# Optimization experiments

Hardware: AMD Instinct MI355X
Metric: run time of the kernel (lower is better)

Reference implementation:

```python
import jax, jax.numpy as jnp
import numpy as np

N = 8192
IN_DIM = 256
HID = 512
NUM_CLASSES = 256
AVG_DEG = 32


def setup_inputs() -> dict:
    key = jax.random.key(0)
    k_a, k_x, k_w1, k_w2 = jax.random.split(key, 4)
    # Binary adjacency with avg degree ~AVG_DEG (entries are exactly 1.0, matching
    # A.nonzero() edge extraction with implicit unit edge weights).
    A = (jax.random.uniform(k_a, (N, N)) < (AVG_DEG / N)).astype(jnp.float32)
    x = jax.random.normal(k_x, (N, IN_DIM), dtype=jnp.float32)
    # GCNConv params: glorot-ish weights, zero bias.
    W1 = jax.random.normal(k_w1, (IN_DIM, HID), dtype=jnp.float32) / np.sqrt(IN_DIM)
    b1 = jnp.zeros((HID,), dtype=jnp.float32)
    W2 = jax.random.normal(k_w2, (HID, NUM_CLASSES), dtype=jnp.float32) / np.sqrt(HID)
    b2 = jnp.zeros((NUM_CLASSES,), dtype=jnp.float32)
    sigmoid_param = jnp.array([10.0], dtype=jnp.float32)
    return {"A": A, "x": x, "W1": W1, "b1": b1, "W2": W2, "b2": b2,
            "sigmoid_param": sigmoid_param}


def _gcn_propagate(A, deg_inv_sqrt, h):
    # PyG GCNConv aggregation with self-loops, without materializing A + I:
    # out_j = d_j^{-1/2} * sum_i A_ij d_i^{-1/2} h_i  +  d_j^{-1} h_j
    m = deg_inv_sqrt[:, None] * h              # [N, d]
    agg = A.T @ m                              # messages flow row -> col
    return deg_inv_sqrt[:, None] * agg + (deg_inv_sqrt[:, None] ** 2) * h


def reference(A, x, W1, b1, W2, b2, sigmoid_param):
    # Degree from column sums of (A + I) — matches gcn_norm's scatter on col.
    deg = jnp.sum(A, axis=0) + 1.0             # [N], >= 1 thanks to self-loop
    deg_inv_sqrt = jax.lax.rsqrt(deg)
    skip_x = x                                  # nn.Identity skip connection
    # GCNConv 1: linear then normalized aggregation, then bias; ReLU.
    h = _gcn_propagate(A, deg_inv_sqrt, x @ W1) + b1
    h = jax.nn.relu(h)
    # GCNConv 2.
    h = _gcn_propagate(A, deg_inv_sqrt, h @ W2) + b2
    # Skip add + scaled sigmoid (original casts to double; kept float32 here).
    return jax.nn.sigmoid(sigmoid_param * (h + skip_x))
```

## Files before the change

kernel.cpp:

```cpp
#include <hip/hip_runtime.h>
#include <hip/hip_bf16.h>

#define N_NODES 8192
#define IN_DIM  256
#define HID     512
#define NCLS    256
#define CAP     128

typedef __attribute__((ext_vector_type(8))) __bf16 bf16x8;
typedef __attribute__((ext_vector_type(4))) float  floatx4;

static __device__ __forceinline__ float bf2f(ushort u) {
    union { float f; unsigned int i; } v; v.i = ((unsigned int)u) << 16; return v.f;
}
static __device__ __forceinline__ ushort f2bf(float f) {
    __hip_bfloat16 b = __float2bfloat16(f);
    return *reinterpret_cast<ushort*>(&b);
}
static __device__ __forceinline__ void bfpair(unsigned int u, float& lo, float& hi) {
    union { float f; unsigned int i; } a, b;
    a.i = u << 16; b.i = u & 0xFFFF0000u;
    lo = a.f; hi = b.f;
}

__global__ __launch_bounds__(256) void build_csc(const float* __restrict__ A,
                                                 int* __restrict__ col_cnt,
                                                 int* __restrict__ col_idx) {
    const int jbase = (blockIdx.x * 256 + threadIdx.x) * 4;
    const int i0 = blockIdx.y * 32;
    for (int ii = 0; ii < 32; ++ii) {
        const int i = i0 + ii;
        const floatx4* p = reinterpret_cast<const floatx4*>(A + (size_t)i * N_NODES + jbase);
        floatx4 v = __builtin_nontemporal_load(p);
        if (v.x != 0.0f) { int q = atomicAdd(&col_cnt[jbase + 0], 1); if (q < CAP) col_idx[(size_t)(jbase + 0) * CAP + q] = i; }
        if (v.y != 0.0f) { int q = atomicAdd(&col_cnt[jbase + 1], 1); if (q < CAP) col_idx[(size_t)(jbase + 1) * CAP + q] = i; }
        if (v.z != 0.0f) { int q = atomicAdd(&col_cnt[jbase + 2], 1); if (q < CAP) col_idx[(size_t)(jbase + 2) * CAP + q] = i; }
        if (v.w != 0.0f) { int q = atomicAdd(&col_cnt[jbase + 3], 1); if (q < CAP) col_idx[(size_t)(jbase + 3) * CAP + q] = i; }
    }
}

__global__ __launch_bounds__(128) void fill_w(const int* __restrict__ col_idx,
                                              const int* __restrict__ col_cnt,
                                              float* __restrict__ w) {
    const int j = blockIdx.x, e = threadIdx.x;
    if (e < min(col_cnt[j], CAP))
        w[(size_t)j * CAP + e] = rsqrtf((float)col_cnt[col_idx[(size_t)j * CAP + e]] + 1.0f);
}

__global__ __launch_bounds__(256) void prep_misc(const float* __restrict__ x,
                                                 const float* __restrict__ W1,
                                                 const float* __restrict__ W2,
                                                 ushort* __restrict__ xb,
                                                 ushort* __restrict__ W1Th, ushort* __restrict__ W1Tl,
                                                 ushort* __restrict__ W2Th, ushort* __restrict__ W2Tl) {
    const int idx = blockIdx.x * 256 + threadIdx.x;
    {
        const int i = idx * 4;
        const floatx4 v = *reinterpret_cast<const floatx4*>(x + i);
        *reinterpret_cast<ushort4*>(xb + i) = ushort4{f2bf(v.x), f2bf(v.y), f2bf(v.z), f2bf(v.w)};
    }
    if (idx < IN_DIM * HID) {
        {
            const int k = idx / HID, n = idx % HID;
            const float v = W1[idx]; const ushort h = f2bf(v);
            W1Th[(size_t)n * IN_DIM + k] = h;
            W1Tl[(size_t)n * IN_DIM + k] = f2bf(v - bf2f(h));
        }
        {
            const int k = idx / NCLS, n = idx % NCLS;
            const float v = W2[idx]; const ushort h = f2bf(v);
            W2Th[(size_t)n * HID + k] = h;
            W2Tl[(size_t)n * HID + k] = f2bf(v - bf2f(h));
        }
    }
}

__global__ __launch_bounds__(256) void agg_x(const ushort* __restrict__ xb,
                                             const int* __restrict__ col_idx,
                                             const int* __restrict__ col_cnt,
                                             const float* __restrict__ w,
                                             ushort* __restrict__ px_hi,
                                             ushort* __restrict__ px_lo) {
    const int j = __builtin_amdgcn_readfirstlane(blockIdx.x * 4 + (threadIdx.x >> 6));
    const int d = (threadIdx.x & 63) * 4;
    const int cntr = col_cnt[j];
    const int cnt = min(cntr, CAP);
    const float dj = rsqrtf((float)cntr + 1.0f);
    float a0, a1, a2, a3;
    {
        const uint2 sv = *reinterpret_cast<const uint2*>(xb + (size_t)j * IN_DIM + d);
        float f0, f1, f2, f3;
        bfpair(sv.x, f0, f1); bfpair(sv.y, f2, f3);
        a0 = dj * f0; a1 = dj * f1; a2 = dj * f2; a3 = dj * f3;
    }
    const int*   __restrict__ lst = col_idx + (size_t)j * CAP;
    const float* __restrict__ wl  = w       + (size_t)j * CAP;
    int e = 0;
    for (; e + 8 <= cnt; e += 8) {
        uint2 rv[8]; float we[8];
#pragma unroll
        for (int q = 0; q < 8; ++q) {
            rv[q] = *reinterpret_cast<const uint2*>(xb + (size_t)lst[e + q] * IN_DIM + d);
            we[q] = wl[e + q];
        }
#pragma unroll
        for (int q = 0; q < 8; ++q) {
            float f0, f1, f2, f3;
            bfpair(rv[q].x, f0, f1); bfpair(rv[q].y, f2, f3);
            a0 += we[q] * f0; a1 += we[q] * f1; a2 += we[q] * f2; a3 += we[q] * f3;
        }
    }
    for (; e < cnt; ++e) {
        const uint2 rv = *reinterpret_cast<const uint2*>(xb + (size_t)lst[e] * IN_DIM + d);
        const float we = wl[e];
        float f0, f1, f2, f3;
        bfpair(rv.x, f0, f1); bfpair(rv.y, f2, f3);
        a0 += we * f0; a1 += we * f1; a2 += we * f2; a3 += we * f3;
    }
    a0 *= dj; a1 *= dj; a2 *= dj; a3 *= dj;
    const ushort h0 = f2bf(a0), h1 = f2bf(a1), h2 = f2bf(a2), h3 = f2bf(a3);
    *reinterpret_cast<ushort4*>(px_hi + (size_t)j * IN_DIM + d) = ushort4{h0, h1, h2, h3};
    *reinterpret_cast<ushort4*>(px_lo + (size_t)j * IN_DIM + d) =
        ushort4{f2bf(a0 - bf2f(h0)), f2bf(a1 - bf2f(h1)), f2bf(a2 - bf2f(h2)), f2bf(a3 - bf2f(h3))};
}

template<int K>
__device__ __forceinline__ void gemm_core(const ushort* __restrict__ Ah,
                                          const ushort* __restrict__ Al,
                                          const ushort* __restrict__ Bh,
                                          const ushort* __restrict__ Bl,
                                          int m_base, int n_base,
                                          int l16, int quad, floatx4 acc[4][2]) {
#pragma unroll 2
    for (int k0 = 0; k0 < K; k0 += 32) {
        const int kf = k0 + quad * 8;
        bf16x8 ah[4], al[4], bh[2], bl[2];
#pragma unroll
        for (int t = 0; t < 4; ++t) {
            const size_t ao = (size_t)(m_base + t * 16 + l16) * K + kf;
            ah[t] = *reinterpret_cast<const bf16x8*>(Ah + ao);
            al[t] = *reinterpret_cast<const bf16x8*>(Al + ao);
        }
#pragma unroll
        for (int t = 0; t < 2; ++t) {
            const size_t bo = (size_t)(n_base + t * 16 + l16) * K + kf;
            bh[t] = *reinterpret_cast<const bf16x8*>(Bh + bo);
            bl[t] = *reinterpret_cast<const bf16x8*>(Bl + bo);
        }
#pragma unroll
        for (int tm = 0; tm < 4; ++tm)
#pragma unroll
            for (int tn = 0; tn < 2; ++tn) {
                acc[tm][tn] = __builtin_amdgcn_mfma_f32_16x16x32_bf16(ah[tm], bl[tn], acc[tm][tn], 0, 0, 0);
                acc[tm][tn] = __builtin_amdgcn_mfma_f32_16x16x32_bf16(al[tm], bh[tn], acc[tm][tn], 0, 0, 0);
                acc[tm][tn] = __builtin_amdgcn_mfma_f32_16x16x32_bf16(ah[tm], bh[tn], acc[tm][tn], 0, 0, 0);
            }
    }
}

__global__ __launch_bounds__(256) void gemm1_fused(const ushort* __restrict__ Ah,
                                                   const ushort* __restrict__ Al,
                                                   const ushort* __restrict__ Bh,
                                                   const ushort* __restrict__ Bl,
                                                   const float* __restrict__ b1,
                                                   ushort* __restrict__ h_hi,
                                                   ushort* __restrict__ h_lo) {
    const int tid = threadIdx.x;
    const int lane = tid & 63, wave = tid >> 6;
    const int wm = wave >> 1, wn = wave & 1;
    const int l16 = lane & 15, quad = lane >> 4;
    const int m_base = blockIdx.x * 128 + wm * 64;
    const int n_base = blockIdx.y * 64 + wn * 32;
    floatx4 acc[4][2] = {};
    gemm_core<IN_DIM>(Ah, Al, Bh, Bl, m_base, n_base, l16, quad, acc);
#pragma unroll
    for (int tn = 0; tn < 2; ++tn) {
        const int col = n_base + tn * 16 + l16;
        const float bv = b1[col];
#pragma unroll
        for (int tm = 0; tm < 4; ++tm)
#pragma unroll
            for (int r = 0; r < 4; ++r) {
                const int row = m_base + tm * 16 + quad * 4 + r;
                const float v = fmaxf(acc[tm][tn][r] + bv, 0.0f);
                const ushort hi = f2bf(v);
                h_hi[(size_t)row * HID + col] = hi;
                h_lo[(size_t)row * HID + col] = f2bf(v - bf2f(hi));
            }
    }
}

__global__ __launch_bounds__(256) void gemm2(const ushort* __restrict__ Ah,
                                             const ushort* __restrict__ Al,
                                             const ushort* __restrict__ Bh,
                                             const ushort* __restrict__ Bl,
                                             ushort* __restrict__ g2b) {
    const int tid = threadIdx.x;
    const int lane = tid & 63, wave = tid >> 6;
    const int wm = wave >> 1, wn = wave & 1;
    const int l16 = lane & 15, quad = lane >> 4;
    const int m_base = blockIdx.x * 128 + wm * 64;
    const int n_base = blockIdx.y * 64 + wn * 32;
    floatx4 acc[4][2] = {};
    gemm_core<HID>(Ah, Al, Bh, Bl, m_base, n_base, l16, quad, acc);
#pragma unroll
    for (int tm = 0; tm < 4; ++tm)
#pragma unroll
        for (int tn = 0; tn < 2; ++tn)
#pragma unroll
            for (int r = 0; r < 4; ++r)
                g2b[(size_t)(m_base + tm * 16 + quad * 4 + r) * NCLS + (n_base + tn * 16 + l16)] =
                    f2bf(acc[tm][tn][r]);
}

__global__ __launch_bounds__(256) void agg_out(const ushort* __restrict__ g2b,
                                               const int* __restrict__ col_idx,
                                               const int* __restrict__ col_cnt,
                                               const float* __restrict__ w,
                                               const float* __restrict__ b2,
                                               const float* __restrict__ x,
                                               const float* __restrict__ sp_p,
                                               float* __restrict__ out) {
    const int j = __builtin_amdgcn_readfirstlane(blockIdx.x * 4 + (threadIdx.x >> 6));
    const int d = (threadIdx.x & 63) * 4;
    const int cntr = col_cnt[j];
    const int cnt = min(cntr, CAP);
    const float dj = rsqrtf((float)cntr + 1.0f);
    float a0, a1, a2, a3;
    {
        const uint2 sv = *reinterpret_cast<const uint2*>(g2b + (size_t)j * NCLS + d);
        float f0, f1, f2, f3;
        bfpair(sv.x, f0, f1); bfpair(sv.y, f2, f3);
        a0 = dj * f0; a1 = dj * f1; a2 = dj * f2; a3 = dj * f3;
    }
    const int*   __restrict__ lst = col_idx + (size_t)j * CAP;
    const float* __restrict__ wl  = w       + (size_t)j * CAP;
    int e = 0;
    for (; e + 8 <= cnt; e += 8) {
        uint2 rv[8]; float we[8];
#pragma unroll
        for (int q = 0; q < 8; ++q) {
            rv[q] = *reinterpret_cast<const uint2*>(g2b + (size_t)lst[e + q] * NCLS + d);
            we[q] = wl[e + q];
        }
#pragma unroll
        for (int q = 0; q < 8; ++q) {
            float f0, f1, f2, f3;
            bfpair(rv[q].x, f0, f1); bfpair(rv[q].y, f2, f3);
            a0 += we[q] * f0; a1 += we[q] * f1; a2 += we[q] * f2; a3 += we[q] * f3;
        }
    }
    for (; e < cnt; ++e) {
        const uint2 rv = *reinterpret_cast<const uint2*>(g2b + (size_t)lst[e] * NCLS + d);
        const float we = wl[e];
        float f0, f1, f2, f3;
        bfpair(rv.x, f0, f1); bfpair(rv.y, f2, f3);
        a0 += we * f0; a1 += we * f1; a2 += we * f2; a3 += we * f3;
    }
    const float sp = sp_p[0];
    const floatx4 bv = *reinterpret_cast<const floatx4*>(b2 + d);
    const floatx4 xv = __builtin_nontemporal_load(
        reinterpret_cast<const floatx4*>(x + (size_t)j * NCLS + d));
    floatx4 o;
    o.x = 1.0f / (1.0f + __expf(-sp * (dj * a0 + bv.x + xv.x)));
    o.y = 1.0f / (1.0f + __expf(-sp * (dj * a1 + bv.y + xv.y)));
    o.z = 1.0f / (1.0f + __expf(-sp * (dj * a2 + bv.z + xv.z)));
    o.w = 1.0f / (1.0f + __expf(-sp * (dj * a3 + bv.w + xv.w)));
    __builtin_nontemporal_store(o, reinterpret_cast<floatx4*>(out + (size_t)j * NCLS + d));
}

extern "C" void kernel_launch(void* const* d_in, const int* in_sizes, int n_in,
                              void* d_out, int out_size, void* d_ws, size_t ws_size,
                              hipStream_t stream) {
    const float* A  = (const float*)d_in[0];
    const float* x  = (const float*)d_in[1];
    const float* W1 = (const float*)d_in[2];
    const float* b1 = (const float*)d_in[3];
    const float* W2 = (const float*)d_in[4];
    const float* b2 = (const float*)d_in[5];
    const float* sp = (const float*)d_in[6];
    float* out = (float*)d_out;

    char* ws = (char*)d_ws;
    size_t off = 0;
    auto alloc = [&](size_t bytes) {
        void* p = ws + off;
        off = (off + bytes + 255) & ~(size_t)255;
        return p;
    };
    int*    col_cnt = (int*)   alloc((size_t)N_NODES * 4);
    int*    col_idx = (int*)   alloc((size_t)N_NODES * CAP * 4);
    float*  wedge   = (float*) alloc((size_t)N_NODES * CAP * 4);
    ushort* xb      = (ushort*)alloc((size_t)N_NODES * IN_DIM * 2);
    ushort* px_hi   = (ushort*)alloc((size_t)N_NODES * IN_DIM * 2);
    ushort* px_lo   = (ushort*)alloc((size_t)N_NODES * IN_DIM * 2);
    ushort* W1Th    = (ushort*)alloc((size_t)HID * IN_DIM * 2);
    ushort* W1Tl    = (ushort*)alloc((size_t)HID * IN_DIM * 2);
    ushort* W2Th    = (ushort*)alloc((size_t)NCLS * HID * 2);
    ushort* W2Tl    = (ushort*)alloc((size_t)NCLS * HID * 2);
    ushort* h_hi    = (ushort*)alloc((size_t)N_NODES * HID * 2);
    ushort* h_lo    = (ushort*)alloc((size_t)N_NODES * HID * 2);
    ushort* g2b     = (ushort*)alloc((size_t)N_NODES * NCLS * 2);

    (void)hipMemsetAsync(col_cnt, 0, (size_t)N_NODES * 4, stream);

    build_csc<<<dim3(8, 256), 256, 0, stream>>>(A, col_cnt, col_idx);
    prep_misc<<<(N_NODES * IN_DIM / 4) / 256, 256, 0, stream>>>(
        x, W1, W2, xb, W1Th, W1Tl, W2Th, W2Tl);
    fill_w<<<N_NODES, 128, 0, stream>>>(col_idx, col_cnt, wedge);

    agg_x<<<N_NODES / 4, 256, 0, stream>>>(xb, col_idx, col_cnt, wedge, px_hi, px_lo);
    gemm1_fused<<<dim3(N_NODES / 128, HID / 64), 256, 0, stream>>>(
        px_hi, px_lo, W1Th, W1Tl, b1, h_hi, h_lo);

    gemm2<<<dim3(N_NODES / 128, NCLS / 64), 256, 0, stream>>>(
        h_hi, h_lo, W2Th, W2Tl, g2b);
    agg_out<<<N_NODES / 4, 256, 0, stream>>>(g2b, col_idx, col_cnt, wedge, b2, x, sp, out);
}
```

Before: 460.2 us.

## Drop activation lo-split, compute degree scales per node, widen GEMM tiles

Result: faster. 434.2 us (-5.6%).

```diff
diff --git a/kernel.cpp b/kernel.cpp
--- a/kernel.cpp
+++ b/kernel.cpp
@@ -25,32 +25,26 @@
 
 __global__ __launch_bounds__(256) void build_csc(const float* __restrict__ A,
                                                  int* __restrict__ col_cnt,
-                                                 int* __restrict__ col_idx) {
+                                                 ushort* __restrict__ col_idx) {
     const int jbase = (blockIdx.x * 256 + threadIdx.x) * 4;
     const int i0 = blockIdx.y * 32;
     for (int ii = 0; ii < 32; ++ii) {
         const int i = i0 + ii;
         const floatx4* p = reinterpret_cast<const floatx4*>(A + (size_t)i * N_NODES + jbase);
         floatx4 v = __builtin_nontemporal_load(p);
-        if (v.x != 0.0f) { int q = atomicAdd(&col_cnt[jbase + 0], 1); if (q < CAP) col_idx[(size_t)(jbase + 0) * CAP + q] = i; }
-        if (v.y != 0.0f) { int q = atomicAdd(&col_cnt[jbase + 1], 1); if (q < CAP) col_idx[(size_t)(jbase + 1) * CAP + q] = i; }
-        if (v.z != 0.0f) { int q = atomicAdd(&col_cnt[jbase + 2], 1); if (q < CAP) col_idx[(size_t)(jbase + 2) * CAP + q] = i; }
-        if (v.w != 0.0f) { int q = atomicAdd(&col_cnt[jbase + 3], 1); if (q < CAP) col_idx[(size_t)(jbase + 3) * CAP + q] = i; }
-    }
-}
-
-__global__ __launch_bounds__(128) void fill_w(const int* __restrict__ col_idx,
-                                              const int* __restrict__ col_cnt,
-                                              float* __restrict__ w) {
-    const int j = blockIdx.x, e = threadIdx.x;
-    if (e < min(col_cnt[j], CAP))
-        w[(size_t)j * CAP + e] = rsqrtf((float)col_cnt[col_idx[(size_t)j * CAP + e]] + 1.0f);
+        if (v.x != 0.0f) { int q = atomicAdd(&col_cnt[jbase + 0], 1); if (q < CAP) col_idx[(size_t)(jbase + 0) * CAP + q] = (ushort)i; }
+        if (v.y != 0.0f) { int q = atomicAdd(&col_cnt[jbase + 1], 1); if (q < CAP) col_idx[(size_t)(jbase + 1) * CAP + q] = (ushort)i; }
+        if (v.z != 0.0f) { int q = atomicAdd(&col_cnt[jbase + 2], 1); if (q < CAP) col_idx[(size_t)(jbase + 2) * CAP + q] = (ushort)i; }
+        if (v.w != 0.0f) { int q = atomicAdd(&col_cnt[jbase + 3], 1); if (q < CAP) col_idx[(size_t)(jbase + 3) * CAP + q] = (ushort)i; }
+    }
 }
 
 __global__ __launch_bounds__(256) void prep_misc(const float* __restrict__ x,
                                                  const float* __restrict__ W1,
                                                  const float* __restrict__ W2,
+                                                 const int* __restrict__ col_cnt,
                                                  ushort* __restrict__ xb,
+                                                 float* __restrict__ dis,
                                                  ushort* __restrict__ W1Th, ushort* __restrict__ W1Tl,
                                                  ushort* __restrict__ W2Th, ushort* __restrict__ W2Tl) {
     const int idx = blockIdx.x * 256 + threadIdx.x;
@@ -59,6 +53,8 @@
         const floatx4 v = *reinterpret_cast<const floatx4*>(x + i);
         *reinterpret_cast<ushort4*>(xb + i) = ushort4{f2bf(v.x), f2bf(v.y), f2bf(v.z), f2bf(v.w)};
     }
+    if (idx < N_NODES)
+        dis[idx] = rsqrtf((float)col_cnt[idx] + 1.0f);
     if (idx < IN_DIM * HID) {
         {
             const int k = idx / HID, n = idx % HID;
@@ -76,16 +72,14 @@
 }
 
 __global__ __launch_bounds__(256) void agg_x(const ushort* __restrict__ xb,
-                                             const int* __restrict__ col_idx,
+                                             const ushort* __restrict__ col_idx,
                                              const int* __restrict__ col_cnt,
-                                             const float* __restrict__ w,
-                                             ushort* __restrict__ px_hi,
-                                             ushort* __restrict__ px_lo) {
+                                             const float* __restrict__ dis,
+                                             ushort* __restrict__ px) {
     const int j = __builtin_amdgcn_readfirstlane(blockIdx.x * 4 + (threadIdx.x >> 6));
     const int d = (threadIdx.x & 63) * 4;
-    const int cntr = col_cnt[j];
-    const int cnt = min(cntr, CAP);
-    const float dj = rsqrtf((float)cntr + 1.0f);
+    const int cnt = min(col_cnt[j], CAP);
+    const float dj = dis[j];
     float a0, a1, a2, a3;
     {
         const uint2 sv = *reinterpret_cast<const uint2*>(xb + (size_t)j * IN_DIM + d);
@@ -93,15 +87,15 @@
         bfpair(sv.x, f0, f1); bfpair(sv.y, f2, f3);
         a0 = dj * f0; a1 = dj * f1; a2 = dj * f2; a3 = dj * f3;
     }
-    const int*   __restrict__ lst = col_idx + (size_t)j * CAP;
-    const float* __restrict__ wl  = w       + (size_t)j * CAP;
+    const ushort* __restrict__ lst = col_idx + (size_t)j * CAP;
     int e = 0;
     for (; e + 8 <= cnt; e += 8) {
         uint2 rv[8]; float we[8];
 #pragma unroll
         for (int q = 0; q < 8; ++q) {
-            rv[q] = *reinterpret_cast<const uint2*>(xb + (size_t)lst[e + q] * IN_DIM + d);
-            we[q] = wl[e + q];
+            const int i = lst[e + q];
+            rv[q] = *reinterpret_cast<const uint2*>(xb + (size_t)i * IN_DIM + d);
+            we[q] = dis[i];
         }
 #pragma unroll
         for (int q = 0; q < 8; ++q) {
@@ -111,38 +105,33 @@
         }
     }
     for (; e < cnt; ++e) {
-        const uint2 rv = *reinterpret_cast<const uint2*>(xb + (size_t)lst[e] * IN_DIM + d);
-        const float we = wl[e];
+        const int i = lst[e];
+        const uint2 rv = *reinterpret_cast<const uint2*>(xb + (size_t)i * IN_DIM + d);
+        const float we = dis[i];
         float f0, f1, f2, f3;
         bfpair(rv.x, f0, f1); bfpair(rv.y, f2, f3);
         a0 += we * f0; a1 += we * f1; a2 += we * f2; a3 += we * f3;
     }
     a0 *= dj; a1 *= dj; a2 *= dj; a3 *= dj;
-    const ushort h0 = f2bf(a0), h1 = f2bf(a1), h2 = f2bf(a2), h3 = f2bf(a3);
-    *reinterpret_cast<ushort4*>(px_hi + (size_t)j * IN_DIM + d) = ushort4{h0, h1, h2, h3};
-    *reinterpret_cast<ushort4*>(px_lo + (size_t)j * IN_DIM + d) =
-        ushort4{f2bf(a0 - bf2f(h0)), f2bf(a1 - bf2f(h1)), f2bf(a2 - bf2f(h2)), f2bf(a3 - bf2f(h3))};
+    *reinterpret_cast<ushort4*>(px + (size_t)j * IN_DIM + d) =
+        ushort4{f2bf(a0), f2bf(a1), f2bf(a2), f2bf(a3)};
 }
 
 template<int K>
-__device__ __forceinline__ void gemm_core(const ushort* __restrict__ Ah,
-                                          const ushort* __restrict__ Al,
+__device__ __forceinline__ void gemm_core(const ushort* __restrict__ A,
                                           const ushort* __restrict__ Bh,
                                           const ushort* __restrict__ Bl,
                                           int m_base, int n_base,
-                                          int l16, int quad, floatx4 acc[4][2]) {
+                                          int l16, int quad, floatx4 acc[4][4]) {
 #pragma unroll 2
     for (int k0 = 0; k0 < K; k0 += 32) {
         const int kf = k0 + quad * 8;
-        bf16x8 ah[4], al[4], bh[2], bl[2];
+        bf16x8 a[4], bh[4], bl[4];
+#pragma unroll
+        for (int t = 0; t < 4; ++t)
+            a[t] = *reinterpret_cast<const bf16x8*>(A + (size_t)(m_base + t * 16 + l16) * K + kf);
 #pragma unroll
         for (int t = 0; t < 4; ++t) {
-            const size_t ao = (size_t)(m_base + t * 16 + l16) * K + kf;
-            ah[t] = *reinterpret_cast<const bf16x8*>(Ah + ao);
-            al[t] = *reinterpret_cast<const bf16x8*>(Al + ao);
-        }
-#pragma unroll
-        for (int t = 0; t < 2; ++t) {
             const size_t bo = (size_t)(n_base + t * 16 + l16) * K + kf;
             bh[t] = *reinterpret_cast<const bf16x8*>(Bh + bo);
             bl[t] = *reinterpret_cast<const bf16x8*>(Bl + bo);
@@ -150,31 +139,28 @@
 #pragma unroll
         for (int tm = 0; tm < 4; ++tm)
 #pragma unroll
-            for (int tn = 0; tn < 2; ++tn) {
-                acc[tm][tn] = __builtin_amdgcn_mfma_f32_16x16x32_bf16(ah[tm], bl[tn], acc[tm][tn], 0, 0, 0);
-                acc[tm][tn] = __builtin_amdgcn_mfma_f32_16x16x32_bf16(al[tm], bh[tn], acc[tm][tn], 0, 0, 0);
-                acc[tm][tn] = __builtin_amdgcn_mfma_f32_16x16x32_bf16(ah[tm], bh[tn], acc[tm][tn], 0, 0, 0);
+            for (int tn = 0; tn < 4; ++tn) {
+                acc[tm][tn] = __builtin_amdgcn_mfma_f32_16x16x32_bf16(a[tm], bl[tn], acc[tm][tn], 0, 0, 0);
+                acc[tm][tn] = __builtin_amdgcn_mfma_f32_16x16x32_bf16(a[tm], bh[tn], acc[tm][tn], 0, 0, 0);
             }
     }
 }
 
-__global__ __launch_bounds__(256) void gemm1_fused(const ushort* __restrict__ Ah,
-                                                   const ushort* __restrict__ Al,
+__global__ __launch_bounds__(256) void gemm1_fused(const ushort* __restrict__ A,
                                                    const ushort* __restrict__ Bh,
                                                    const ushort* __restrict__ Bl,
                                                    const float* __restrict__ b1,
-                                                   ushort* __restrict__ h_hi,
-                                                   ushort* __restrict__ h_lo) {
+                                                   ushort* __restrict__ h) {
     const int tid = threadIdx.x;
     const int lane = tid & 63, wave = tid >> 6;
     const int wm = wave >> 1, wn = wave & 1;
     const int l16 = lane & 15, quad = lane >> 4;
     const int m_base = blockIdx.x * 128 + wm * 64;
-    const int n_base = blockIdx.y * 64 + wn * 32;
-    floatx4 acc[4][2] = {};
-    gemm_core<IN_DIM>(Ah, Al, Bh, Bl, m_base, n_base, l16, quad, acc);
-#pragma unroll
-    for (int tn = 0; tn < 2; ++tn) {
+    const int n_base = blockIdx.y * 128 + wn * 64;
+    floatx4 acc[4][4] = {};
+    gemm_core<IN_DIM>(A, Bh, Bl, m_base, n_base, l16, quad, acc);
+#pragma unroll
+    for (int tn = 0; tn < 4; ++tn) {
         const int col = n_base + tn * 16 + l16;
         const float bv = b1[col];
 #pragma unroll
@@ -182,16 +168,12 @@
 #pragma unroll
             for (int r = 0; r < 4; ++r) {
                 const int row = m_base + tm * 16 + quad * 4 + r;
-                const float v = fmaxf(acc[tm][tn][r] + bv, 0.0f);
-                const ushort hi = f2bf(v);
-                h_hi[(size_t)row * HID + col] = hi;
-                h_lo[(size_t)row * HID + col] = f2bf(v - bf2f(hi));
+                h[(size_t)row * HID + col] = f2bf(fmaxf(acc[tm][tn][r] + bv, 0.0f));
             }
     }
 }
 
-__global__ __launch_bounds__(256) void gemm2(const ushort* __restrict__ Ah,
-                                             const ushort* __restrict__ Al,
+__global__ __launch_bounds__(256) void gemm2(const ushort* __restrict__ A,
                                              const ushort* __restrict__ Bh,
                                              const ushort* __restrict__ Bl,
                                              ushort* __restrict__ g2b) {
@@ -200,13 +182,13 @@
     const int wm = wave >> 1, wn = wave & 1;
     const int l16 = lane & 15, quad = lane >> 4;
     const int m_base = blockIdx.x * 128 + wm * 64;
-    const int n_base = blockIdx.y * 64 + wn * 32;
-    floatx4 acc[4][2] = {};
-    gemm_core<HID>(Ah, Al, Bh, Bl, m_base, n_base, l16, quad, acc);
+    const int n_base = blockIdx.y * 128 + wn * 64;
+    floatx4 acc[4][4] = {};
+    gemm_core<HID>(A, Bh, Bl, m_base, n_base, l16, quad, acc);
 #pragma unroll
     for (int tm = 0; tm < 4; ++tm)
 #pragma unroll
-        for (int tn = 0; tn < 2; ++tn)
+        for (int tn = 0; tn < 4; ++tn)
 #pragma unroll
             for (int r = 0; r < 4; ++r)
                 g2b[(size_t)(m_base + tm * 16 + quad * 4 + r) * NCLS + (n_base + tn * 16 + l16)] =
@@ -214,18 +196,17 @@
 }
 
 __global__ __launch_bounds__(256) void agg_out(const ushort* __restrict__ g2b,
-                                               const int* __restrict__ col_idx,
+                                               const ushort* __restrict__ col_idx,
                                                const int* __restrict__ col_cnt,
-                                               const float* __restrict__ w,
+                                               const float* __restrict__ dis,
                                                const float* __restrict__ b2,
                                                const float* __restrict__ x,
                                                const float* __restrict__ sp_p,
                                                float* __restrict__ out) {
     const int j = __builtin_amdgcn_readfirstlane(blockIdx.x * 4 + (threadIdx.x >> 6));
     const int d = (threadIdx.x & 63) * 4;
-    const int cntr = col_cnt[j];
-    const int cnt = min(cntr, CAP);
-    const float dj = rsqrtf((float)cntr + 1.0f);
+    const int cnt = min(col_cnt[j], CAP);
+    const float dj = dis[j];
     float a0, a1, a2, a3;
     {
         const uint2 sv = *reinterpret_cast<const uint2*>(g2b + (size_t)j * NCLS + d);
@@ -233,15 +214,15 @@
         bfpair(sv.x, f0, f1); bfpair(sv.y, f2, f3);
         a0 = dj * f0; a1 = dj * f1; a2 = dj * f2; a3 = dj * f3;
     }
-    const int*   __restrict__ lst = col_idx + (size_t)j * CAP;
-    const float* __restrict__ wl  = w       + (size_t)j * CAP;
+    const ushort* __restrict__ lst = col_idx + (size_t)j * CAP;
     int e = 0;
     for (; e + 8 <= cnt; e += 8) {
         uint2 rv[8]; float we[8];
 #pragma unroll
         for (int q = 0; q < 8; ++q) {
-            rv[q] = *reinterpret_cast<const uint2*>(g2b + (size_t)lst[e + q] * NCLS + d);
-            we[q] = wl[e + q];
+            const int i = lst[e + q];
+            rv[q] = *reinterpret_cast<const uint2*>(g2b + (size_t)i * NCLS + d);
+            we[q] = dis[i];
         }
 #pragma unroll
         for (int q = 0; q < 8; ++q) {
@@ -251,8 +232,9 @@
         }
     }
     for (; e < cnt; ++e) {
-        const uint2 rv = *reinterpret_cast<const uint2*>(g2b + (size_t)lst[e] * NCLS + d);
-        const float we = wl[e];
+        const int i = lst[e];
+        const uint2 rv = *reinterpret_cast<const uint2*>(g2b + (size_t)i * NCLS + d);
+        const float we = dis[i];
         float f0, f1, f2, f3;
         bfpair(rv.x, f0, f1); bfpair(rv.y, f2, f3);
         a0 += we * f0; a1 += we * f1; a2 += we * f2; a3 += we * f3;
@@ -289,31 +271,28 @@
         return p;
     };
     int*    col_cnt = (int*)   alloc((size_t)N_NODES * 4);
-    int*    col_idx = (int*)   alloc((size_t)N_NODES * CAP * 4);
-    float*  wedge   = (float*) alloc((size_t)N_NODES * CAP * 4);
+    float*  dis     = (float*) alloc((size_t)N_NODES * 4);
+    ushort* col_idx = (ushort*)alloc((size_t)N_NODES * CAP * 2);
     ushort* xb      = (ushort*)alloc((size_t)N_NODES * IN_DIM * 2);
-    ushort* px_hi   = (ushort*)alloc((size_t)N_NODES * IN_DIM * 2);
-    ushort* px_lo   = (ushort*)alloc((size_t)N_NODES * IN_DIM * 2);
+    ushort* px      = (ushort*)alloc((size_t)N_NODES * IN_DIM * 2);
     ushort* W1Th    = (ushort*)alloc((size_t)HID * IN_DIM * 2);
     ushort* W1Tl    = (ushort*)alloc((size_t)HID * IN_DIM * 2);
     ushort* W2Th    = (ushort*)alloc((size_t)NCLS * HID * 2);
     ushort* W2Tl    = (ushort*)alloc((size_t)NCLS * HID * 2);
-    ushort* h_hi    = (ushort*)alloc((size_t)N_NODES * HID * 2);
-    ushort* h_lo    = (ushort*)alloc((size_t)N_NODES * HID * 2);
+    ushort* h       = (ushort*)alloc((size_t)N_NODES * HID * 2);
     ushort* g2b     = (ushort*)alloc((size_t)N_NODES * NCLS * 2);
 
     (void)hipMemsetAsync(col_cnt, 0, (size_t)N_NODES * 4, stream);
 
     build_csc<<<dim3(8, 256), 256, 0, stream>>>(A, col_cnt, col_idx);
     prep_misc<<<(N_NODES * IN_DIM / 4) / 256, 256, 0, stream>>>(
-        x, W1, W2, xb, W1Th, W1Tl, W2Th, W2Tl);
-    fill_w<<<N_NODES, 128, 0, stream>>>(col_idx, col_cnt, wedge);
-
-    agg_x<<<N_NODES / 4, 256, 0, stream>>>(xb, col_idx, col_cnt, wedge, px_hi, px_lo);
-    gemm1_fused<<<dim3(N_NODES / 128, HID / 64), 256, 0, stream>>>(
-        px_hi, px_lo, W1Th, W1Tl, b1, h_hi, h_lo);
-
-    gemm2<<<dim3(N_NODES / 128, NCLS / 64), 256, 0, stream>>>(
-        h_hi, h_lo, W2Th, W2Tl, g2b);
-    agg_out<<<N_NODES / 4, 256, 0, stream>>>(g2b, col_idx, col_cnt, wedge, b2, x, sp, out);
-}
+        x, W1, W2, col_cnt, xb, dis, W1Th, W1Tl, W2Th, W2Tl);
+
+    agg_x<<<N_NODES / 4, 256, 0, stream>>>(xb, col_idx, col_cnt, dis, px);
+    gemm1_fused<<<dim3(N_NODES / 128, HID / 128), 256, 0, stream>>>(
+        px, W1Th, W1Tl, b1, h);
+
+    gemm2<<<dim3(N_NODES / 128, NCLS / 128), 256, 0, stream>>>(
+        h, W2Th, W2Tl, g2b);
+    agg_out<<<N_NODES / 4, 256, 0, stream>>>(g2b, col_idx, col_cnt, dis, b2, x, sp, out);
+}
```
